# Performance work log

Hardware: AMD Instinct MI355X
Metric: run time of the kernel (lower is better)

## Reference

```python
import jax, jax.numpy as jnp
import numpy as np

B, T, C, H, E, K, F = 2, 2048, 1024, 16, 8, 2, 2048  # batch, seq, d_model, heads, experts, top_k, d_ffn
EPS = 1e-5


def setup_inputs() -> dict:
    key = jax.random.key(0)
    ks = jax.random.split(key, 6)
    s = 0.02
    return {
        "x": jax.random.normal(ks[0], (B, T, C), jnp.float32),
        "ln1_w": jnp.ones((C,), jnp.float32),
        "c_attn_w": jax.random.normal(ks[1], (C, 3 * C), jnp.float32) * s,
        "c_proj_w": jax.random.normal(ks[2], (C, C), jnp.float32) * s,
        "ln2_w": jnp.ones((C,), jnp.float32),
        "router_w": jax.random.normal(ks[3], (C, E), jnp.float32) * s,
        "w1": jnp.clip(jax.random.normal(ks[4], (C, E * F), jnp.float32) * s, -0.06, 0.06),
        "w2": jnp.clip(jax.random.normal(ks[5], (E * F, C), jnp.float32) * s, -0.06, 0.06),
    }


def layernorm(x, w):
    m = x.mean(-1, keepdims=True)
    v = x.var(-1, keepdims=True)
    return (x - m) * jax.lax.rsqrt(v + EPS) * w


def attention(x, c_attn_w, c_proj_w):
    b, t, c = x.shape
    hd = c // H
    q, k, v = jnp.split(x @ c_attn_w, 3, axis=-1)
    q = q.reshape(b, t, H, hd).transpose(0, 2, 1, 3)  # bhtd
    k = k.reshape(b, t, H, hd).transpose(0, 2, 1, 3)
    v = v.reshape(b, t, H, hd).transpose(0, 2, 1, 3)
    att = jnp.einsum('bhqd,bhkd->bhqk', q, k) / jnp.sqrt(jnp.asarray(hd, x.dtype))
    causal = jnp.tril(jnp.ones((t, t), bool))
    att = jnp.where(causal, att, jnp.asarray(-jnp.inf, att.dtype))
    att = jax.nn.softmax(att, axis=-1)
    y = jnp.einsum('bhqk,bhkd->bhqd', att, v)
    y = y.transpose(0, 2, 1, 3).reshape(b, t, c)
    return y @ c_proj_w


def moe_mlp(x, router_w, w1, w2):
    b, t, c = x.shape
    xf = x.reshape(-1, c)  # (N, C), N = b*t
    router_logits = xf @ router_w  # (N, E)
    probs = jax.nn.softmax(router_logits.astype(jnp.float32), axis=-1)
    rw, sel = jax.lax.top_k(probs, K)  # (N, K)
    rw = rw / rw.sum(axis=-1, keepdims=True)  # norm_topk_prob=True
    rw = rw.astype(x.dtype)
    # expert e uses w1[:, e*F:(e+1)*F] and w2[e*F:(e+1)*F, :]
    w1e = w1.reshape(c, E, F).transpose(1, 0, 2)  # (E, C, F)
    w2e = w2.reshape(E, F, c)  # (E, F, C)
    h = jax.nn.gelu(jnp.einsum('nc,ecf->enf', xf, w1e), approximate=False)
    y_all = jnp.einsum('enf,efc->nec', h, w2e)  # (N, E, C)
    y_sel = jnp.take_along_axis(y_all, sel[:, :, None], axis=1)  # (N, K, C)
    y = (y_sel * rw[:, :, None]).sum(axis=1)
    return y.reshape(b, t, c)


def reference(x, ln1_w, c_attn_w, c_proj_w, ln2_w, router_w, w1, w2):
    x = x + attention(layernorm(x, ln1_w), c_attn_w, c_proj_w)
    x = x + moe_mlp(layernorm(x, ln2_w), router_w, w1, w2)
    return x
```

## Files before the change

### kernel.cpp

```cpp
#include <hip/hip_runtime.h>
#include <hip/hip_bf16.h>

#define BB 2
#define TT 2048
#define CCH 1024
#define HH 16
#define HD 64
#define EE 8
#define FF 2048
#define NTOK (BB*TT)

typedef __bf16 bf16x8 __attribute__((ext_vector_type(8)));
typedef float f32x4 __attribute__((ext_vector_type(4)));
typedef unsigned int u32;
typedef const u32 __attribute__((address_space(1)))* gads;
typedef u32 __attribute__((address_space(3)))* lads;

static __device__ __forceinline__ unsigned short f2bf(float f) {
  union { float f; unsigned u; } v; v.f = f;
  unsigned u = v.u;
  u += 0x7fffu + ((u >> 16) & 1u);
  return (unsigned short)(u >> 16);
}
static __device__ __forceinline__ float bf2f(unsigned short h) {
  union { unsigned u; float f; } v; v.u = ((unsigned)h) << 16;
  return v.f;
}

__global__ __launch_bounds__(256) void k_transpose(const float* __restrict__ in,
    unsigned short* __restrict__ out, int R, int Cc) {
  __shared__ float tile[32][33];
  size_t zoff = (size_t)blockIdx.z * (size_t)R * (size_t)Cc;
  int r0 = blockIdx.y * 32, c0 = blockIdx.x * 32;
  int tx = threadIdx.x, ty = threadIdx.y;
#pragma unroll
  for (int ii = 0; ii < 4; ++ii) {
    int i = ty + ii * 8;
    tile[i][tx] = in[zoff + (size_t)(r0 + i) * Cc + c0 + tx];
  }
  __syncthreads();
#pragma unroll
  for (int ii = 0; ii < 4; ++ii) {
    int i = ty + ii * 8;
    out[zoff + (size_t)(c0 + i) * R + r0 + tx] = f2bf(tile[tx][i]);
  }
}

__global__ __launch_bounds__(256) void k_ln(const float* __restrict__ x,
    const float* __restrict__ w, unsigned short* __restrict__ out) {
  int row = blockIdx.x;
  const float* xr = x + (size_t)row * CCH;
  int tid = threadIdx.x;
  float4 v = *(const float4*)&xr[tid * 4];
  float s = v.x + v.y + v.z + v.w;
  float ss = v.x * v.x + v.y * v.y + v.z * v.z + v.w * v.w;
#pragma unroll
  for (int off = 32; off; off >>= 1) { s += __shfl_xor(s, off); ss += __shfl_xor(ss, off); }
  __shared__ float red[8];
  int wv = tid >> 6, l = tid & 63;
  if (l == 0) { red[wv] = s; red[4 + wv] = ss; }
  __syncthreads();
  s = red[0] + red[1] + red[2] + red[3];
  ss = red[4] + red[5] + red[6] + red[7];
  float mean = s * (1.f / CCH);
  float var = ss * (1.f / CCH) - mean * mean;
  float inv = rsqrtf(var + 1e-5f);
  float4 w4 = *(const float4*)&w[tid * 4];
  ushort4 o;
  o.x = f2bf((v.x - mean) * inv * w4.x);
  o.y = f2bf((v.y - mean) * inv * w4.y);
  o.z = f2bf((v.z - mean) * inv * w4.z);
  o.w = f2bf((v.w - mean) * inv * w4.w);
  *(ushort4*)&out[(size_t)row * CCH + tid * 4] = o;
}

__global__ __launch_bounds__(256) void k_ln2_router(const float* __restrict__ x,
    const float* __restrict__ w, const float* __restrict__ rw,
    unsigned short* __restrict__ out, int* __restrict__ sel,
    float* __restrict__ selw) {
  int row = blockIdx.x;
  const float* xr = x + (size_t)row * CCH;
  int tid = threadIdx.x;
  float4 v = *(const float4*)&xr[tid * 4];
  float s = v.x + v.y + v.z + v.w;
  float ss = v.x * v.x + v.y * v.y + v.z * v.z + v.w * v.w;
#pragma unroll
  for (int off = 32; off; off >>= 1) { s += __shfl_xor(s, off); ss += __shfl_xor(ss, off); }
  __shared__ float red[8];
  __shared__ float red2[4][8];
  int wv = tid >> 6, l = tid & 63;
  if (l == 0) { red[wv] = s; red[4 + wv] = ss; }
  __syncthreads();
  s = red[0] + red[1] + red[2] + red[3];
  ss = red[4] + red[5] + red[6] + red[7];
  float mean = s * (1.f / CCH);
  float var = ss * (1.f / CCH) - mean * mean;
  float inv = rsqrtf(var + 1e-5f);
  float4 w4 = *(const float4*)&w[tid * 4];
  float nv0 = (v.x - mean) * inv * w4.x;
  float nv1 = (v.y - mean) * inv * w4.y;
  float nv2 = (v.z - mean) * inv * w4.z;
  float nv3 = (v.w - mean) * inv * w4.w;
  ushort4 o;
  o.x = f2bf(nv0); o.y = f2bf(nv1); o.z = f2bf(nv2); o.w = f2bf(nv3);
  *(ushort4*)&out[(size_t)row * CCH + tid * 4] = o;
  const float* rr = rw + (size_t)tid * 4 * EE;
  float lg[8];
#pragma unroll
  for (int e = 0; e < 8; ++e)
    lg[e] = nv0 * rr[e] + nv1 * rr[8 + e] + nv2 * rr[16 + e] + nv3 * rr[24 + e];
#pragma unroll
  for (int e = 0; e < 8; ++e) {
    float t = lg[e];
#pragma unroll
    for (int off = 32; off; off >>= 1) t += __shfl_xor(t, off);
    lg[e] = t;
  }
  if (l == 0) {
#pragma unroll
    for (int e = 0; e < 8; ++e) red2[wv][e] = lg[e];
  }
  __syncthreads();
  if (tid == 0) {
    float logit[8];
#pragma unroll
    for (int e = 0; e < 8; ++e)
      logit[e] = red2[0][e] + red2[1][e] + red2[2][e] + red2[3][e];
    float m1 = logit[0]; int i1 = 0;
#pragma unroll
    for (int e = 1; e < 8; ++e) if (logit[e] > m1) { m1 = logit[e]; i1 = e; }
    float m2 = -INFINITY; int i2 = 0;
#pragma unroll
    for (int e = 0; e < 8; ++e) if (e != i1 && logit[e] > m2) { m2 = logit[e]; i2 = e; }
    float w1v = 1.f / (1.f + __expf(m2 - m1));
    sel[row * 2] = i1; sel[row * 2 + 1] = i2;
    selw[row * 2] = w1v; selw[row * 2 + 1] = 1.f - w1v;
  }
}

#define CSP 140
#define CFP 70
template<int EPI>
__global__ __launch_bounds__(256, 4) void k_gemm128(
    const unsigned short* __restrict__ A, const unsigned short* __restrict__ BT,
    unsigned short* __restrict__ Cb, float* __restrict__ Cf,
    const float* __restrict__ resid, int M, int N, int K,
    const int* __restrict__ tokarr, const int* __restrict__ slotarr,
    const float* __restrict__ wgtarr, const int* __restrict__ offs,
    const int* __restrict__ counts, const int* __restrict__ tmap)
{
  __shared__ __align__(16) char pool[35840];
  unsigned short* As = (unsigned short*)pool;
  unsigned short* Bs = (unsigned short*)(pool + 16384);

  int mb, nb, e = 0, off = 0, cnt = M;
  if (EPI >= 2) {
    int tm = blockIdx.x;
    if (tm >= tmap[8]) return;
    e = 0;
    while (tm >= tmap[e + 1]) ++e;
    mb = tm - tmap[e];
    nb = blockIdx.y;
    cnt = counts[e]; off = offs[e];
  } else {
    int gx = gridDim.x, gy = gridDim.y;
    int nwg = gx * gy;
    int orig = blockIdx.y * gx + blockIdx.x;
    int q = nwg >> 3, r = nwg & 7;
    int xcd = orig & 7, idx = orig >> 3;
    int wk = (xcd < r ? xcd * (q + 1) : r * (q + 1) + (xcd - r) * q) + idx;
    nb = wk % gy; mb = wk / gy;
  }
  int m0 = mb * 128, n0 = nb * 128;

  int tid = threadIdx.x, l = tid & 63, w = tid >> 6;
  int scol = (((l & 7) ^ ((l >> 3) & 7)) * 8);
  const unsigned short* aptr[4];
  const unsigned short* bptr[4];
  const unsigned short* bbase = BT + (size_t)e * (size_t)N * K;
#pragma unroll
  for (int i = 0; i < 4; ++i) {
    int row = (w * 4 + i) * 8 + (l >> 3);
    int ra;
    if (EPI == 2)      ra = tokarr[off + min(m0 + row, cnt - 1)];
    else if (EPI == 3) ra = off + min(m0 + row, cnt - 1);
    else               ra = m0 + row;
    aptr[i] = A + (size_t)ra * K + scol;
    bptr[i] = bbase + (size_t)(n0 + row) * K + scol;
  }

  int wr = (w >> 1) * 64, wc = (w & 1) * 64;
  int frow = l & 15;
  int fkB = (l >> 4) * 16;
  int swz = (frow & 7) << 4;
  f32x4 acc[4][4] = {};

  for (int k0 = 0; k0 < K; k0 += 64) {
#pragma unroll
    for (int i = 0; i < 4; ++i) {
      int j = w * 4 + i;
      __builtin_amdgcn_global_load_lds((gads)(const void*)(aptr[i] + k0),
                                       (lads)(void*)(As + j * 512), 16, 0, 0);
      __builtin_amdgcn_global_load_lds((gads)(const void*)(bptr[i] + k0),
                                       (lads)(void*)(Bs + j * 512), 16, 0, 0);
    }
    __syncthreads();
    const char* ab = (const char*)As;
    const char* bb = (const char*)Bs;
#pragma unroll
    for (int kk = 0; kk < 2; ++kk) {
      int inr = (kk * 64 + fkB) ^ swz;
      bf16x8 af[4], bfr[4];
#pragma unroll
      for (int mi = 0; mi < 4; ++mi)
        af[mi] = *(const bf16x8*)(ab + (wr + mi * 16 + frow) * 128 + inr);
#pragma unroll
      for (int ni = 0; ni < 4; ++ni)
        bfr[ni] = *(const bf16x8*)(bb + (wc + ni * 16 + frow) * 128 + inr);
#pragma unroll
      for (int mi = 0; mi < 4; ++mi)
#pragma unroll
        for (int ni = 0; ni < 4; ++ni)
          acc[mi][ni] = __builtin_amdgcn_mfma_f32_16x16x32_bf16(af[mi], bfr[ni],
                                                                acc[mi][ni], 0, 0, 0);
    }
    __syncthreads();
  }

  int g4 = (l >> 4) * 4, cl = l & 15;

  if (EPI == 0 || EPI == 2 || EPI == 3) {
    unsigned short* Cs = (unsigned short*)pool;
#pragma unroll
    for (int mi = 0; mi < 4; ++mi)
#pragma unroll
      for (int ni = 0; ni < 4; ++ni)
#pragma unroll
        for (int r2 = 0; r2 < 4; ++r2) {
          float v = acc[mi][ni][r2];
          if (EPI == 2) {
            float u2 = 1.5957691216f * v * (1.f + 0.044715f * v * v);
            float ex = __expf(u2);
            v = v - v / (ex + 1.f);
          }
          Cs[(wr + mi * 16 + g4 + r2) * CSP + wc + ni * 16 + cl] = f2bf(v);
        }
    __syncthreads();
    int row = tid >> 1, c0 = (tid & 1) * 64;
    if (EPI == 0 || m0 + row < cnt) {
      if (EPI == 3) {
        int fl = off + m0 + row;
        int tok = tokarr[fl], slot = slotarr[fl];
        float wg = wgtarr[fl];
        unsigned short* dst = Cb + ((size_t)tok * 2 + slot) * N + n0 + c0;
#pragma unroll
        for (int j = 0; j < 8; ++j) {
          uint4 pk = *(const uint4*)&Cs[row * CSP + c0 + j * 8];
          unsigned short* sp = (unsigned short*)&pk;
          ushort4 o0, o1;
          o0.x = f2bf(bf2f(sp[0]) * wg); o0.y = f2bf(bf2f(sp[1]) * wg);
          o0.z = f2bf(bf2f(sp[2]) * wg); o0.w = f2bf(bf2f(sp[3]) * wg);
          o1.x = f2bf(bf2f(sp[4]) * wg); o1.y = f2bf(bf2f(sp[5]) * wg);
          o1.z = f2bf(bf2f(sp[6]) * wg); o1.w = f2bf(bf2f(sp[7]) * wg);
          *(ushort4*)&dst[j * 8] = o0;
          *(ushort4*)&dst[j * 8 + 4] = o1;
        }
      } else {
        size_t grow = (EPI == 2) ? (size_t)(off + m0 + row) : (size_t)(m0 + row);
        unsigned short* dst = Cb + grow * N + n0 + c0;
#pragma unroll
        for (int j = 0; j < 8; ++j)
          ((uint4*)dst)[j] = *(const uint4*)&Cs[row * CSP + c0 + j * 8];
      }
    }
  } else {
    float* Csf = (float*)pool;
#pragma unroll
    for (int p = 0; p < 2; ++p) {
      __syncthreads();
      if ((w & 1) == p) {
#pragma unroll
        for (int mi = 0; mi < 4; ++mi)
#pragma unroll
          for (int ni = 0; ni < 4; ++ni)
#pragma unroll
            for (int r2 = 0; r2 < 4; ++r2)
              Csf[(wr + mi * 16 + g4 + r2) * CFP + ni * 16 + cl] = acc[mi][ni][r2];
      }
      __syncthreads();
      int row = tid >> 1, c0 = (tid & 1) * 32;
      int gcol = n0 + p * 64 + c0;
      float* dst = Cf + (size_t)(m0 + row) * N + gcol;
      const float* rsd = resid + (size_t)(m0 + row) * N + gcol;
#pragma unroll
      for (int j = 0; j < 8; ++j) {
        float4 v = *(const float4*)&Csf[row * CFP + c0 + j * 4];
        float4 rr = ((const float4*)rsd)[j];
        v.x += rr.x; v.y += rr.y; v.z += rr.z; v.w += rr.w;
        ((float4*)dst)[j] = v;
      }
    }
  }
}

__global__ __launch_bounds__(256) void k_attn_mfma(const unsigned short* __restrict__ qkv,
    unsigned short* __restrict__ yout)
{
  int fblk = blockIdx.x;
  int xcd = fblk & 7, s = fblk >> 3;
  int hb = s & 3;
  int h = xcd + 8 * (hb & 1);
  int b = hb >> 1;
  int t = s >> 2, t0 = t & 7, u = t >> 3;
  int qt = (u == 0) ? t0 : (u == 1) ? (15 - t0) : (u == 2) ? (16 + t0) : (31 - t0);
  int q0 = qt * 64;

  int tid = threadIdx.x, l = tid & 63, w = tid >> 6;
  const size_t rs = 3 * CCH;

  __shared__ __align__(16) unsigned short Ks[64][72];
  __shared__ __align__(16) unsigned short VtL[64 * 72];
  __shared__ __align__(16) unsigned short Ps[4][16][72];

  int frow = l & 15, fk = (l >> 4) * 8;
  int g4 = l >> 4;
  int kr = tid >> 2, kc0 = (tid & 3) * 8;
  int vr = tid >> 2, vc0 = (tid & 3) * 16;
  int vphys = (((vr >> 3) + 2 * (tid & 3)) & 7) * 8 + (vr & 7);

  const unsigned short* qp = qkv + (size_t)((size_t)b * TT + q0 + w * 16 + frow) * rs + h * HD;
  bf16x8 qf0 = *(const bf16x8*)&qp[fk];
  bf16x8 qf1 = *(const bf16x8*)&qp[32 + fk];

  f32x4 oacc[4] = {};
  float mrow[4] = {-INFINITY, -INFINITY, -INFINITY, -INFINITY};
  float lrow[4] = {};

  uint4 rk0, rk1, rv0, rv1;
  {
    const unsigned short* kp = qkv + (size_t)((size_t)b * TT + kr) * rs + CCH + h * HD;
    rk0 = *(const uint4*)&kp[kc0];
    rk1 = *(const uint4*)&kp[kc0 + 32];
    const unsigned short* vp = qkv + (size_t)((size_t)b * TT + vr) * rs + 2 * CCH + h * HD + vc0;
    rv0 = *(const uint4*)&vp[0];
    rv1 = *(const uint4*)&vp[8];
  }

  for (int kb = 0; kb <= qt; ++kb) {
    __syncthreads();
    *(uint4*)&Ks[kr][kc0]      = rk0;
    *(uint4*)&Ks[kr][kc0 + 32] = rk1;
    {
      unsigned short tmp[16];
      *(uint4*)&tmp[0] = rv0; *(uint4*)&tmp[8] = rv1;
#pragma unroll
      for (int j = 0; j < 16; ++j) VtL[(vc0 + j) * 72 + vphys] = tmp[j];
    }
    __syncthreads();
    if (kb < qt) {
      int k0n = (kb + 1) * 64;
      const unsigned short* kp = qkv + (size_t)((size_t)b * TT + k0n + kr) * rs + CCH + h * HD;
      rk0 = *(const uint4*)&kp[kc0];
      rk1 = *(const uint4*)&kp[kc0 + 32];
      const unsigned short* vp = qkv + (size_t)((size_t)b * TT + k0n + vr) * rs + 2 * CCH + h * HD + vc0;
      rv0 = *(const uint4*)&vp[0];
      rv1 = *(const uint4*)&vp[8];
    }

    f32x4 sacc[4] = {};
    __builtin_amdgcn_s_setprio(1);
#pragma unroll
    for (int nb = 0; nb < 4; ++nb) {
      bf16x8 kf0 = *(const bf16x8*)&Ks[nb * 16 + frow][fk];
      bf16x8 kf1 = *(const bf16x8*)&Ks[nb * 16 + frow][32 + fk];
      sacc[nb] = __builtin_amdgcn_mfma_f32_16x16x32_bf16(qf0, kf0, sacc[nb], 0, 0, 0);
      sacc[nb] = __builtin_amdgcn_mfma_f32_16x16x32_bf16(qf1, kf1, sacc[nb], 0, 0, 0);
    }
    __builtin_amdgcn_s_setprio(0);

    bool diag = (kb == qt);
    float sv[4][4];
#pragma unroll
    for (int nb = 0; nb < 4; ++nb)
#pragma unroll
      for (int r = 0; r < 4; ++r) {
        float v = sacc[nb][r] * 0.125f;
        if (diag) {
          int ckv = nb * 16 + frow;
          int rq = w * 16 + 4 * g4 + r;
          if (ckv > rq) v = -INFINITY;
        }
        sv[nb][r] = v;
      }
    float fscale[4];
#pragma unroll
    for (int r = 0; r < 4; ++r) {
      float vm = fmaxf(fmaxf(sv[0][r], sv[1][r]), fmaxf(sv[2][r], sv[3][r]));
      vm = fmaxf(vm, __shfl_xor(vm, 1));
      vm = fmaxf(vm, __shfl_xor(vm, 2));
      vm = fmaxf(vm, __shfl_xor(vm, 4));
      vm = fmaxf(vm, __shfl_xor(vm, 8));
      float mnew = fmaxf(mrow[r], vm);
      float f = __expf(mrow[r] - mnew);
      mrow[r] = mnew;
      fscale[r] = f;
      float psum = 0.f;
#pragma unroll
      for (int nb = 0; nb < 4; ++nb) {
        float p = __expf(sv[nb][r] - mnew);
        sv[nb][r] = p;
        psum += p;
      }
      psum += __shfl_xor(psum, 1);
      psum += __shfl_xor(psum, 2);
      psum += __shfl_xor(psum, 4);
      psum += __shfl_xor(psum, 8);
      lrow[r] = lrow[r] * f + psum;
    }
#pragma unroll
    for (int nb = 0; nb < 4; ++nb)
#pragma unroll
      for (int r = 0; r < 4; ++r) {
        oacc[nb][r] *= fscale[r];
        Ps[w][4 * g4 + r][nb * 16 + frow] = f2bf(sv[nb][r]);
      }
    __builtin_amdgcn_s_setprio(1);
#pragma unroll
    for (int ks = 0; ks < 2; ++ks) {
      bf16x8 pa = *(const bf16x8*)&Ps[w][frow][ks * 32 + fk];
#pragma unroll
      for (int nb = 0; nb < 4; ++nb) {
        int vchunk = ((ks * 4 + (l >> 4) + 2 * nb) & 7) * 8;
        bf16x8 vb = *(const bf16x8*)&VtL[(nb * 16 + frow) * 72 + vchunk];
        oacc[nb] = __builtin_amdgcn_mfma_f32_16x16x32_bf16(pa, vb, oacc[nb], 0, 0, 0);
      }
    }
    __builtin_amdgcn_s_setprio(0);
  }

  unsigned short* yo = yout + (size_t)((size_t)b * TT + q0 + w * 16) * CCH + h * HD;
#pragma unroll
  for (int r = 0; r < 4; ++r) {
    float inv = 1.f / lrow[r];
    int row = 4 * g4 + r;
#pragma unroll
    for (int nb = 0; nb < 4; ++nb)
      yo[(size_t)row * CCH + nb * 16 + frow] = f2bf(oacc[nb][r] * inv);
  }
}

__global__ __launch_bounds__(256) void k_count(const int* __restrict__ sel,
    int* __restrict__ counts_pad)
{
  __shared__ int hist[8];
  int tid = threadIdx.x;
  if (tid < 8) hist[tid] = 0;
  __syncthreads();
  int i = blockIdx.x * 256 + tid;
  atomicAdd(&hist[sel[i]], 1);
  __syncthreads();
  if (tid < 8) atomicAdd(&counts_pad[tid * 16], hist[tid]);
}

__global__ void k_offsets(const int* __restrict__ counts_pad, int* __restrict__ counts,
                          int* __restrict__ offs, int* __restrict__ cursors_pad,
                          int* __restrict__ tmap) {
  if (threadIdx.x == 0 && blockIdx.x == 0) {
    int acc = 0, t = 0;
    tmap[0] = 0;
    for (int e = 0; e < 8; ++e) {
      int c = counts_pad[e * 16];
      counts[e] = c; offs[e] = acc; cursors_pad[e * 16] = acc; acc += c;
      t += (c + 127) >> 7;
      tmap[e + 1] = t;
    }
  }
}

__global__ __launch_bounds__(256) void k_scatter(const int* __restrict__ sel,
    const float* __restrict__ selw, int* __restrict__ cursors_pad,
    int* __restrict__ tokarr, int* __restrict__ slotarr, float* __restrict__ wgtarr)
{
  int t = blockIdx.x * 256 + threadIdx.x;
  int l = threadIdx.x & 63;
#pragma unroll
  for (int s2 = 0; s2 < 2; ++s2) {
    int e = sel[t * 2 + s2];
    int pos = 0;
#pragma unroll
    for (int ex = 0; ex < 8; ++ex) {
      unsigned long long mask = __ballot(e == ex);
      if (e == ex) {
        int leader = __ffsll((long long)mask) - 1;
        int cntw = __popcll(mask);
        int base = 0;
        if (l == leader) base = atomicAdd(&cursors_pad[ex * 16], cntw);
        base = __shfl(base, leader);
        unsigned long long below = (l == 0) ? 0ull : (mask << (64 - l));
        pos = base + __popcll(below);
      }
    }
    tokarr[pos] = t; slotarr[pos] = s2; wgtarr[pos] = selw[t * 2 + s2];
  }
}

__global__ __launch_bounds__(256) void k_combine(const float* __restrict__ x2,
    const unsigned short* __restrict__ ypb, float* __restrict__ out)
{
  int i = blockIdx.x * 256 + threadIdx.x;
  int n = i >> 7, cw = i & 127;
  float4 a0 = ((const float4*)x2)[i * 2];
  float4 a1 = ((const float4*)x2)[i * 2 + 1];
  uint4 y0p = *(const uint4*)&ypb[((size_t)n * 2) * CCH + cw * 8];
  uint4 y1p = *(const uint4*)&ypb[((size_t)n * 2 + 1) * CCH + cw * 8];
  const unsigned short* y0 = (const unsigned short*)&y0p;
  const unsigned short* y1 = (const unsigned short*)&y1p;
  float4 o0, o1;
  o0.x = a0.x + bf2f(y0[0]) + bf2f(y1[0]);
  o0.y = a0.y + bf2f(y0[1]) + bf2f(y1[1]);
  o0.z = a0.z + bf2f(y0[2]) + bf2f(y1[2]);
  o0.w = a0.w + bf2f(y0[3]) + bf2f(y1[3]);
  o1.x = a1.x + bf2f(y0[4]) + bf2f(y1[4]);
  o1.y = a1.y + bf2f(y0[5]) + bf2f(y1[5]);
  o1.z = a1.z + bf2f(y0[6]) + bf2f(y1[6]);
  o1.w = a1.w + bf2f(y0[7]) + bf2f(y1[7]);
  ((float4*)out)[i * 2] = o0;
  ((float4*)out)[i * 2 + 1] = o1;
}

extern "C" void kernel_launch(void* const* d_in, const int* in_sizes, int n_in,
                              void* d_out, int out_size, void* d_ws, size_t ws_size,
                              hipStream_t stream) {
  const float* x     = (const float*)d_in[0];
  const float* ln1w  = (const float*)d_in[1];
  const float* attnw = (const float*)d_in[2];
  const float* projw = (const float*)d_in[3];
  const float* ln2w  = (const float*)d_in[4];
  const float* routw = (const float*)d_in[5];
  const float* w1    = (const float*)d_in[6];
  const float* w2    = (const float*)d_in[7];
  char* ws = (char*)d_ws;

  unsigned short* attn_wT = (unsigned short*)(ws + 0);
  unsigned short* proj_wT = (unsigned short*)(ws + 6291456);
  unsigned short* w1T     = (unsigned short*)(ws + 8388608);
  unsigned short* w2T     = (unsigned short*)(ws + 41943040);
  unsigned short* xn      = (unsigned short*)(ws + 75497472);
  unsigned short* qkv     = (unsigned short*)(ws + 83886080);
  unsigned short* yattn   = (unsigned short*)(ws + 109051904);
  unsigned short* hbuf    = (unsigned short*)(ws + 83886080);
  float* x2 = (float*)(ws + 117440512);
  unsigned short* ypb = (unsigned short*)(ws + 134217728);
  char* rbase = ws + 167772160;
  int* counts_pad  = (int*)(rbase);
  int* counts      = (int*)(rbase + 512);
  int* cursors_pad = (int*)(rbase + 1024);
  int* offs        = (int*)(rbase + 1536);
  int* tmap        = (int*)(rbase + 1600);
  int* sel         = (int*)(rbase + 2048);
  float* selw      = (float*)(rbase + 2048 + 32768);
  int* tokarr      = (int*)(rbase + 2048 + 65536);
  int* slotarr     = (int*)(rbase + 2048 + 98304);
  float* wgtarr    = (float*)(rbase + 2048 + 131072);
  float* outp = (float*)d_out;

  hipMemsetAsync(counts_pad, 0, 512, stream);

  dim3 tb(32, 8);
  k_transpose<<<dim3(96, 32, 1), tb, 0, stream>>>(attnw, attn_wT, 1024, 3072);
  k_transpose<<<dim3(32, 32, 1), tb, 0, stream>>>(projw, proj_wT, 1024, 1024);
  k_transpose<<<dim3(512, 32, 1), tb, 0, stream>>>(w1, w1T, 1024, 16384);
  k_transpose<<<dim3(32, 64, 8), tb, 0, stream>>>(w2, w2T, 2048, 1024);

  k_ln<<<NTOK, 256, 0, stream>>>(x, ln1w, xn);
  k_gemm128<0><<<dim3(32, 24), 256, 0, stream>>>(xn, attn_wT, qkv, nullptr, nullptr,
      NTOK, 3 * CCH, CCH, nullptr, nullptr, nullptr, nullptr, nullptr, nullptr);
  k_attn_mfma<<<dim3(1024), 256, 0, stream>>>(qkv, yattn);
  k_gemm128<1><<<dim3(32, 8), 256, 0, stream>>>(yattn, proj_wT, nullptr, x2, x,
      NTOK, CCH, CCH, nullptr, nullptr, nullptr, nullptr, nullptr, nullptr);
  k_ln2_router<<<NTOK, 256, 0, stream>>>(x2, ln2w, routw, xn, sel, selw);
  k_count<<<32, 256, 0, stream>>>(sel, counts_pad);
  k_offsets<<<1, 64, 0, stream>>>(counts_pad, counts, offs, cursors_pad, tmap);
  k_scatter<<<NTOK / 256, 256, 0, stream>>>(sel, selw, cursors_pad, tokarr, slotarr, wgtarr);
  k_gemm128<2><<<dim3(72, 16), 256, 0, stream>>>(xn, w1T, hbuf, nullptr, nullptr,
      NTOK, FF, CCH, tokarr, slotarr, wgtarr, offs, counts, tmap);
  k_gemm128<3><<<dim3(72, 8), 256, 0, stream>>>(hbuf, w2T, ypb, nullptr, nullptr,
      NTOK, CCH, FF, tokarr, slotarr, wgtarr, offs, counts, tmap);
  k_combine<<<2048, 256, 0, stream>>>(x2, ypb, outp);
}
```

Baseline: 379.1 us.

## Split long causal attention tiles across two blocks and merge partials

Query tiles 16-31, which have the longest causal KV ranges, are now split into two halves processed by separate blocks. A lookup table sets the order of work items. Each half writes unnormalized fp32 partial outputs plus the running max and sum into scratch space reused from x2, and a new merge kernel combines them with log-sum-exp rescaling. This is meant to shorten the tail caused by long diagonal tiles and improve load balance across CUs. The cost is an extra kernel launch and extra fp32 partial traffic.

```diff
diff --git a/kernel.cpp b/kernel.cpp
--- a/kernel.cpp
+++ b/kernel.cpp
@@ -303,16 +303,27 @@
   }
 }
 
+__device__ const unsigned char g_witab[48] = {
+  124,125,120, 62, 121,116,117,112, 58, 113,108,109,104, 54,
+  105,100,101, 96, 50,  97, 92, 93, 88, 46,  89, 84, 85, 80, 42,
+   81, 76, 77, 72, 38,  73, 68, 69, 64, 34,  65, 30, 26, 22, 18, 14, 10, 6, 2
+};
+
 __global__ __launch_bounds__(256) void k_attn_mfma(const unsigned short* __restrict__ qkv,
-    unsigned short* __restrict__ yout)
+    unsigned short* __restrict__ yout, float* __restrict__ Opart, float* __restrict__ ml)
 {
   int fblk = blockIdx.x;
   int xcd = fblk & 7, s = fblk >> 3;
-  int hb = s & 3;
-  int h = xcd + 8 * (hb & 1);
-  int b = hb >> 1;
-  int t = s >> 2, t0 = t & 7, u = t >> 3;
-  int qt = (u == 0) ? t0 : (u == 1) ? (15 - t0) : (u == 2) ? (16 + t0) : (31 - t0);
+  int hbl = s & 3;
+  int h = xcd + 8 * (hbl & 1);
+  int b = hbl >> 1;
+  int item = s >> 2;
+  int v = g_witab[item];
+  int qt = v >> 2, code = v & 3;
+  bool split = (code != 2);
+  int h1 = (qt + 2) >> 1;
+  int kb0 = (code == 1) ? h1 : 0;
+  int kb1 = (code == 0) ? h1 : (qt + 1);
   int q0 = qt * 64;
 
   int tid = threadIdx.x, l = tid & 63, w = tid >> 6;
@@ -338,15 +349,16 @@
 
   uint4 rk0, rk1, rv0, rv1;
   {
-    const unsigned short* kp = qkv + (size_t)((size_t)b * TT + kr) * rs + CCH + h * HD;
+    int k0 = kb0 * 64;
+    const unsigned short* kp = qkv + (size_t)((size_t)b * TT + k0 + kr) * rs + CCH + h * HD;
     rk0 = *(const uint4*)&kp[kc0];
     rk1 = *(const uint4*)&kp[kc0 + 32];
-    const unsigned short* vp = qkv + (size_t)((size_t)b * TT + vr) * rs + 2 * CCH + h * HD + vc0;
+    const unsigned short* vp = qkv + (size_t)((size_t)b * TT + k0 + vr) * rs + 2 * CCH + h * HD + vc0;
     rv0 = *(const uint4*)&vp[0];
     rv1 = *(const uint4*)&vp[8];
   }
 
-  for (int kb = 0; kb <= qt; ++kb) {
+  for (int kb = kb0; kb < kb1; ++kb) {
     __syncthreads();
     *(uint4*)&Ks[kr][kc0]      = rk0;
     *(uint4*)&Ks[kr][kc0 + 32] = rk1;
@@ -357,7 +369,7 @@
       for (int j = 0; j < 16; ++j) VtL[(vc0 + j) * 72 + vphys] = tmp[j];
     }
     __syncthreads();
-    if (kb < qt) {
+    if (kb + 1 < kb1) {
       int k0n = (kb + 1) * 64;
       const unsigned short* kp = qkv + (size_t)((size_t)b * TT + k0n + kr) * rs + CCH + h * HD;
       rk0 = *(const uint4*)&kp[kc0];
@@ -384,13 +396,13 @@
     for (int nb = 0; nb < 4; ++nb)
 #pragma unroll
       for (int r = 0; r < 4; ++r) {
-        float v = sacc[nb][r] * 0.125f;
+        float vv = sacc[nb][r] * 0.125f;
         if (diag) {
           int ckv = nb * 16 + frow;
           int rq = w * 16 + 4 * g4 + r;
-          if (ckv > rq) v = -INFINITY;
+          if (ckv > rq) vv = -INFINITY;
         }
-        sv[nb][r] = v;
+        sv[nb][r] = vv;
       }
     float fscale[4];
 #pragma unroll
@@ -438,14 +450,69 @@
     __builtin_amdgcn_s_setprio(0);
   }
 
-  unsigned short* yo = yout + (size_t)((size_t)b * TT + q0 + w * 16) * CCH + h * HD;
-#pragma unroll
-  for (int r = 0; r < 4; ++r) {
-    float inv = 1.f / lrow[r];
-    int row = 4 * g4 + r;
-#pragma unroll
-    for (int nb = 0; nb < 4; ++nb)
-      yo[(size_t)row * CCH + nb * 16 + frow] = f2bf(oacc[nb][r] * inv);
+  if (!split) {
+    unsigned short* yo = yout + (size_t)((size_t)b * TT + q0 + w * 16) * CCH + h * HD;
+#pragma unroll
+    for (int r = 0; r < 4; ++r) {
+      float inv = 1.f / lrow[r];
+      int row = 4 * g4 + r;
+#pragma unroll
+      for (int nb = 0; nb < 4; ++nb)
+        yo[(size_t)row * CCH + nb * 16 + frow] = f2bf(oacc[nb][r] * inv);
+    }
+  } else {
+    int hbg = b * HH + h;
+    int pid = hbg * 16 + (qt - 16);
+    int part = pid * 2 + code;
+    float* Op = Opart + (size_t)part * 4096;
+#pragma unroll
+    for (int r = 0; r < 4; ++r) {
+      int row = w * 16 + 4 * g4 + r;
+#pragma unroll
+      for (int nb = 0; nb < 4; ++nb)
+        Op[row * 64 + nb * 16 + frow] = oacc[nb][r];
+    }
+    if (frow == 0) {
+      float* mlp = ml + (size_t)part * 128;
+#pragma unroll
+      for (int r = 0; r < 4; ++r) {
+        int row = w * 16 + 4 * g4 + r;
+        mlp[row] = mrow[r];
+        mlp[64 + row] = lrow[r];
+      }
+    }
+  }
+}
+
+__global__ __launch_bounds__(256) void k_attn_merge(const float* __restrict__ Opart,
+    const float* __restrict__ ml, unsigned short* __restrict__ yout)
+{
+  int pid = blockIdx.x;
+  int hbg = pid >> 4;
+  int qt = 16 + (pid & 15);
+  int b = hbg >> 4, h = hbg & 15;
+  int tid = threadIdx.x;
+  int row = tid >> 2, c0 = (tid & 3) * 16;
+  const float* mlA = ml + (size_t)(pid * 2) * 128;
+  const float* mlB = mlA + 128;
+  float mA = mlA[row], lA = mlA[64 + row];
+  float mB = mlB[row], lB = mlB[64 + row];
+  float m = fmaxf(mA, mB);
+  float fA = __expf(mA - m), fB = __expf(mB - m);
+  float inv = 1.f / (lA * fA + lB * fB);
+  const float* OA = Opart + (size_t)(pid * 2) * 4096 + row * 64 + c0;
+  const float* OB = OA + 4096;
+  unsigned short* yo = yout + ((size_t)b * TT + qt * 64 + row) * CCH + h * HD + c0;
+#pragma unroll
+  for (int j4 = 0; j4 < 4; ++j4) {
+    float4 a = *(const float4*)&OA[j4 * 4];
+    float4 bb = *(const float4*)&OB[j4 * 4];
+    ushort4 o;
+    o.x = f2bf((a.x * fA + bb.x * fB) * inv);
+    o.y = f2bf((a.y * fA + bb.y * fB) * inv);
+    o.z = f2bf((a.z * fA + bb.z * fB) * inv);
+    o.w = f2bf((a.w * fA + bb.w * fB) * inv);
+    *(ushort4*)&yo[j4 * 4] = o;
   }
 }
 
@@ -550,6 +617,8 @@
   unsigned short* yattn   = (unsigned short*)(ws + 109051904);
   unsigned short* hbuf    = (unsigned short*)(ws + 83886080);
   float* x2 = (float*)(ws + 117440512);
+  float* Opart = x2;
+  float* mlbuf = x2 + 4194304;
   unsigned short* ypb = (unsigned short*)(ws + 134217728);
   char* rbase = ws + 167772160;
   int* counts_pad  = (int*)(rbase);
@@ -575,7 +644,8 @@
   k_ln<<<NTOK, 256, 0, stream>>>(x, ln1w, xn);
   k_gemm128<0><<<dim3(32, 24), 256, 0, stream>>>(xn, attn_wT, qkv, nullptr, nullptr,
       NTOK, 3 * CCH, CCH, nullptr, nullptr, nullptr, nullptr, nullptr, nullptr);
-  k_attn_mfma<<<dim3(1024), 256, 0, stream>>>(qkv, yattn);
+  k_attn_mfma<<<dim3(1536), 256, 0, stream>>>(qkv, yattn, Opart, mlbuf);
+  k_attn_merge<<<dim3(512), 256, 0, stream>>>(Opart, mlbuf, yattn);
   k_gemm128<1><<<dim3(32, 8), 256, 0, stream>>>(yattn, proj_wT, nullptr, x2, x,
       NTOK, CCH, CCH, nullptr, nullptr, nullptr, nullptr, nullptr, nullptr);
   k_ln2_router<<<NTOK, 256, 0, stream>>>(x2, ln2w, routw, xn, sel, selw);
```

Measured after the change: 372.2 us. About the same (-1.8%).
